# Kernel optimization log

Measured on AMD Instinct MI355X. Metric: run time of the kernel, lower is better.

## Reference

```python
import jax, jax.numpy as jnp
import numpy as np

N, E, D, H, C = 50000, 1600000, 128, 2, 32

def setup_inputs() -> dict:
    key = jax.random.key(0)
    ks = jax.random.split(key, 8)
    x = jax.random.normal(ks[0], (N, D), jnp.float32)
    edge_index = jax.random.randint(ks[1], (2, E), 0, N)
    intra_enrichment_weights = jax.random.uniform(ks[2], (E,), jnp.float32)
    W = jax.random.normal(ks[3], (D, H * C), jnp.float32) * (1.0 / np.sqrt(D))
    att_src = jax.random.normal(ks[4], (H, C), jnp.float32) * 0.1
    att_dst = jax.random.normal(ks[5], (H, C), jnp.float32) * 0.1
    bias = jnp.zeros((H * C,), jnp.float32)
    enrichment_scale = jnp.asarray(0.01, jnp.float32)
    return dict(x=x, edge_index=edge_index,
                intra_enrichment_weights=intra_enrichment_weights,
                W=W, att_src=att_src, att_dst=att_dst, bias=bias,
                enrichment_scale=enrichment_scale)

def reference(x, edge_index, intra_enrichment_weights, W, att_src, att_dst, bias, enrichment_scale):
    n = x.shape[0]
    xf = jax.nn.elu(x)                       # F.elu on input features
    h = (xf @ W).reshape(n, H, C)            # [N, heads, out]
    # GATConv default add_self_loops=True
    loop = jnp.arange(n, dtype=edge_index.dtype)
    src = jnp.concatenate([edge_index[0], loop])
    dst = jnp.concatenate([edge_index[1], loop])
    a_src = jnp.einsum('nhc,hc->nh', h, att_src)   # [N, H]
    a_dst = jnp.einsum('nhc,hc->nh', h, att_dst)
    alpha = jax.nn.leaky_relu(a_src[src] + a_dst[dst], 0.2)  # [E+N, H]
    # softmax over incoming edges per destination node
    m = jax.ops.segment_max(alpha, dst, num_segments=n)
    e = jnp.exp(alpha - m[dst])
    denom = jax.ops.segment_sum(e, dst, num_segments=n)
    p = e / denom[dst]                       # every node has a self-loop -> denom > 0
    out = jax.ops.segment_sum(h[src] * p[:, :, None], dst, num_segments=n)  # [N, H, C]
    out = out.reshape(n, H * C) + bias
    # enrichment bias (scatter-mean of per-edge weights over source nodes)
    s0 = edge_index[0]
    nw = jax.ops.segment_sum(intra_enrichment_weights, s0, num_segments=n)
    cnt = jax.ops.segment_sum(jnp.ones_like(intra_enrichment_weights), s0, num_segments=n)
    nw = nw / jnp.maximum(cnt, 1.0)
    nw = jnp.clip(nw, 0.2, 5.0)
    scale_factor = 0.1 * jax.nn.sigmoid(enrichment_scale)
    return out + scale_factor * (nw[:, None] - 1.0)
```

## Files before the change

kernel.cpp:

```cpp
#include <hip/hip_runtime.h>


typedef unsigned int u32;
typedef unsigned short u16;

#define SLOTS2 2624
#define NB2_MAX 800
#define EPB 4096

#define XS 136
#define CS 68

#define SMEM_F 34816

typedef __attribute__((ext_vector_type(8))) short short8;
typedef __attribute__((ext_vector_type(4))) float float4v;

__device__ __forceinline__ u16 f2bf(float f) {
    union { float f; u32 u; } v; v.f = f;
    u32 r = v.u + 0x7fffu + ((v.u >> 16) & 1u);
    return (u16)(r >> 16);
}
__device__ __forceinline__ float bf2f(u16 u) {
    union { u32 i; float f; } v; v.i = ((u32)u) << 16; return v.f;
}
__device__ __forceinline__ float bf_lo(u32 u) {
    union { u32 i; float f; } v; v.i = u << 16; return v.f;
}
__device__ __forceinline__ float bf_hi(u32 u) {
    union { u32 i; float f; } v; v.i = u & 0xFFFF0000u; return v.f;
}
__device__ __forceinline__ void bf_split(float v, short& hi, short& lo) {
    u16 h = f2bf(v);
    float hf = bf2f(h);
    hi = (short)h;
    lo = (short)f2bf(v - hf);
}

__global__ void k_prep(const float* __restrict__ Wm,
                       short* __restrict__ Whf, short* __restrict__ Wlf)
{
    int t = threadIdx.x;
    for (int p = t; p < 1024; p += 256) {
        int frag = p >> 6, l = p & 63;
        int ks = frag >> 2, nt = frag & 3;
        int q = l >> 4, m = l & 15;
        int f = nt * 16 + m;
#pragma unroll
        for (int j = 0; j < 8; ++j) {
            int k = ks * 32 + q * 8 + j;
            float wv = Wm[k * 64 + f];
            short hi, lo; bf_split(wv, hi, lo);
            Whf[p * 8 + j] = hi;
            Wlf[p * 8 + j] = lo;
        }
    }
}

static __device__ __forceinline__ void node_body(
    char* smem, int nb_id,
    const float* __restrict__ x,
    const short* __restrict__ Whf, const short* __restrict__ Wlf,
    const float* __restrict__ att_s, const float* __restrict__ att_d,
    u32* __restrict__ hb32, float* __restrict__ a_src, float* __restrict__ a_dst,
    int nN)
{
    short* Ah = (short*)smem;
    short* Al = (short*)(smem + 17408);
    float* Cl = (float*)Ah;

    int t = threadIdx.x;
    int n0 = nb_id * 64;

    for (int j = 0; j < 8; ++j) {
        int idx = t + 256 * j;
        int r = idx >> 5, c4 = idx & 31;
        int gn = n0 + r;
        float4 xv = make_float4(0.f, 0.f, 0.f, 0.f);
        if (gn < nN) xv = ((const float4*)x)[(size_t)gn * 32 + c4];
        float e[4];
        e[0] = xv.x > 0.f ? xv.x : __expf(xv.x) - 1.f;
        e[1] = xv.y > 0.f ? xv.y : __expf(xv.y) - 1.f;
        e[2] = xv.z > 0.f ? xv.z : __expf(xv.z) - 1.f;
        e[3] = xv.w > 0.f ? xv.w : __expf(xv.w) - 1.f;
        short h4[4], l4[4];
#pragma unroll
        for (int i = 0; i < 4; ++i) bf_split(e[i], h4[i], l4[i]);
        *(short4*)&Ah[r * XS + c4 * 4] = make_short4(h4[0], h4[1], h4[2], h4[3]);
        *(short4*)&Al[r * XS + c4 * 4] = make_short4(l4[0], l4[1], l4[2], l4[3]);
    }
    __syncthreads();

    {
        int w = t >> 6, l = t & 63;
        int q = l >> 4, m = l & 15;
        int arow = w * 16 + m;
        float4v acc[4] = {};
#pragma unroll
        for (int ks = 0; ks < 4; ++ks) {
            int k0 = ks * 32 + q * 8;
            short8 ah = *(const short8*)&Ah[arow * XS + k0];
            short8 al = *(const short8*)&Al[arow * XS + k0];
#pragma unroll
            for (int nt = 0; nt < 4; ++nt) {
                short8 bh = *(const short8*)&Whf[((ks * 4 + nt) * 64 + l) * 8];
                short8 bl = *(const short8*)&Wlf[((ks * 4 + nt) * 64 + l) * 8];
                acc[nt] = __builtin_amdgcn_mfma_f32_16x16x32_bf16(ah, bh, acc[nt], 0, 0, 0);
                acc[nt] = __builtin_amdgcn_mfma_f32_16x16x32_bf16(ah, bl, acc[nt], 0, 0, 0);
                acc[nt] = __builtin_amdgcn_mfma_f32_16x16x32_bf16(al, bh, acc[nt], 0, 0, 0);
            }
        }
        __syncthreads();
#pragma unroll
        for (int nt = 0; nt < 4; ++nt)
#pragma unroll
            for (int r = 0; r < 4; ++r)
                Cl[(w * 16 + q * 4 + r) * CS + nt * 16 + m] = acc[nt][r];
    }
    __syncthreads();

    {
        int nl = t >> 2, fq = t & 3;
        int gn = n0 + nl;
        float ps = 0.f, pd = 0.f;
        if (gn < nN) {
            float hv[16];
#pragma unroll
            for (int i = 0; i < 16; ++i) {
                int f = fq * 16 + i;
                hv[i] = Cl[nl * CS + f];
                ps = fmaf(hv[i], att_s[f], ps);
                pd = fmaf(hv[i], att_d[f], pd);
            }
#pragma unroll
            for (int i = 0; i < 8; ++i) {
                u32 pk = ((u32)f2bf(hv[2 * i + 1]) << 16) | (u32)f2bf(hv[2 * i]);
                hb32[(size_t)gn * 32 + fq * 8 + i] = pk;
            }
        }
        float ps2 = ps + __shfl_xor(ps, 1, 64);
        float pd2 = pd + __shfl_xor(pd, 1, 64);
        if (gn < nN && (fq & 1) == 0) {
            a_src[2 * gn + (fq >> 1)] = ps2;
            a_dst[2 * gn + (fq >> 1)] = pd2;
        }
    }
}

static __device__ __forceinline__ void partA_body(
    char* smem, int pa_id,
    const int* __restrict__ ei, const float* __restrict__ wgt,
    int* cursA, int* cursB, u32* bufA, u32* bufB, int E, int nb2)
{
    u32* arr  = (u32*)smem;
    int* cnt  = (int*)(smem + 16384);
    int* lofs = (int*)(smem + 19584);
    int* bas  = (int*)(smem + 22784);
    int* part = (int*)(smem + 25984);

    int t = threadIdx.x;
    int base = pa_id * EPB;
    int nv = min(EPB, E - base);
    int sv[16], dv[16]; float wv[16];
#pragma unroll
    for (int k = 0; k < 16; ++k) {
        int e = base + k * 256 + t;
        if (e < E) { sv[k] = ei[e]; dv[k] = ei[E + e]; wv[k] = wgt[e]; }
        else       { sv[k] = -1;    dv[k] = -1;        wv[k] = 0.f; }
    }

#pragma unroll
    for (int side = 0; side < 2; ++side) {
        int* curs = side ? cursB : cursA;
        u32* buf  = side ? bufB  : bufA;

        for (int b = t; b < nb2; b += 256) cnt[b] = 0;
        __syncthreads();
#pragma unroll
        for (int k = 0; k < 16; ++k) {
            int key = side ? sv[k] : dv[k];
            if (key >= 0) atomicAdd(&cnt[key >> 6], 1);
        }
        __syncthreads();
        for (int b = t; b < nb2; b += 256) {
            int c = cnt[b];
            if (c > 0) bas[b] = atomicAdd(&curs[b], c);
        }
        __syncthreads();
        {
            int c[4]; int s = 0;
#pragma unroll
            for (int i = 0; i < 4; ++i) {
                int bb = 4 * t + i;
                c[i] = (bb < nb2) ? cnt[bb] : 0;
                s += c[i];
            }
            part[t] = s;
            __syncthreads();
            for (int off = 1; off < 256; off <<= 1) {
                int v = (t >= off) ? part[t - off] : 0;
                __syncthreads();
                part[t] += v;
                __syncthreads();
            }
            int excl = part[t] - s;
#pragma unroll
            for (int i = 0; i < 4; ++i) {
                int bb = 4 * t + i;
                if (bb < nb2) lofs[bb] = excl;
                excl += c[i];
            }
        }
        __syncthreads();
        for (int b = t; b < nb2; b += 256) cnt[b] = 0;
        __syncthreads();
#pragma unroll
        for (int k = 0; k < 16; ++k) {
            int key = side ? sv[k] : dv[k];
            if (key >= 0) {
                int bk = key >> 6;
                int r = lofs[bk] + atomicAdd(&cnt[bk], 1);
                u32 payload;
                if (side) {
                    u32 wq = (u32)(wv[k] * 65536.f);
                    if (wq > 0xFFFFu) wq = 0xFFFFu;
                    payload = ((u32)(key & 63) << 16) | wq;
                } else {
                    payload = ((u32)(key & 63) << 16) | (u32)sv[k];
                }
                arr[r] = ((u32)bk << 22) | payload;
            }
        }
        __syncthreads();
        for (int i = t; i < nv; i += 256) {
            u32 va = arr[i];
            int bk = va >> 22;
            int g = bas[bk] + (i - lofs[bk]);
            if (g < SLOTS2) buf[(size_t)bk * SLOTS2 + g] = va & 0x3FFFFFu;
        }
        __syncthreads();
    }
}

__global__ __launch_bounds__(256) void k_fused(
    const float* __restrict__ x,
    const short* __restrict__ Whf, const short* __restrict__ Wlf,
    const float* __restrict__ att_s, const float* __restrict__ att_d,
    u32* __restrict__ hb32, float* __restrict__ a_src, float* __restrict__ a_dst,
    const int* __restrict__ ei, const float* __restrict__ wgt,
    int* cursA, int* cursB, u32* bufA, u32* bufB,
    int E, int nb2, int nblkA, int nN)
{
    __shared__ __align__(16) char smem[SMEM_F];
    int bid = blockIdx.x;
    int q3 = bid / 3;
    if ((bid % 3) == 0 && q3 < nblkA) {
        partA_body(smem, q3, ei, wgt, cursA, cursB, bufA, bufB, E, nb2);
    } else {
        int npa_before = min(q3 + ((bid % 3) ? 1 : 0), nblkA);
        node_body(smem, bid - npa_before, x, Whf, Wlf, att_s, att_d,
                  hb32, a_src, a_dst, nN);
    }
}

__global__ __launch_bounds__(512) void k_final(
    const u32* __restrict__ hb32,
    const float* __restrict__ a_src, const float* __restrict__ a_dst,
    const u32* __restrict__ bufA, const int* __restrict__ cursA,
    const u32* __restrict__ bufB, const int* __restrict__ cursB,
    const float* __restrict__ bias, const float* __restrict__ esc,
    float* __restrict__ out, int nN)
{
    __shared__ u32 st[SLOTS2];
    __shared__ u16 st2[SLOTS2];
    __shared__ int ldeg[64], lscan[64], lcur[64];
    __shared__ int usum[64], ucnt[64];

    int b = blockIdx.x, t = threadIdx.x;
    int n0 = b << 6;
    int nA = cursA[b]; if (nA > SLOTS2) nA = SLOTS2;
    int nB = cursB[b]; if (nB > SLOTS2) nB = SLOTS2;

    if (t < 64) { ldeg[t] = 0; lcur[t] = 0; usum[t] = 0; ucnt[t] = 0; }
    __syncthreads();
    for (int i = t; i < nA; i += 512) {
        u32 v = bufA[(size_t)b * SLOTS2 + i];
        st[i] = v;
        atomicAdd(&ldeg[v >> 16], 1);
    }
    for (int i = t; i < nB; i += 512) {
        u32 v = bufB[(size_t)b * SLOTS2 + i];
        atomicAdd(&usum[v >> 16], (int)(v & 0xFFFFu));
        atomicAdd(&ucnt[v >> 16], 1);
    }
    __syncthreads();
    if (t < 64) lscan[t] = ldeg[t];
    __syncthreads();
    for (int off = 1; off < 64; off <<= 1) {
        int v = 0;
        if (t < 64 && t >= off) v = lscan[t - off];
        __syncthreads();
        if (t < 64) lscan[t] += v;
        __syncthreads();
    }
    if (t < 64) lscan[t] -= ldeg[t];
    __syncthreads();
    for (int i = t; i < nA; i += 512) {
        u32 v = st[i];
        int dl = v >> 16;
        int pos = lscan[dl] + atomicAdd(&lcur[dl], 1);
        st2[pos] = (u16)(v & 0xFFFFu);
    }
    __syncthreads();

    int ws = t >> 6, lane = t & 63;
    int q = lane >> 4, fl = lane & 15, head = fl >> 3;
    const uint2* hb2 = (const uint2*)hb32;
    float escv = esc[0];
    float sf = 0.1f / (1.f + __expf(-escv));
    float4 bb = ((const float4*)bias)[fl];

    for (int dl = ws; dl < 64; dl += 8) {
        int gn = n0 + dl;
        if (gn >= nN) break;
        int beg = lscan[dl], cnt = ldeg[dl];
        float2 adv = ((const float2*)a_dst)[gn];
        float2 asv = ((const float2*)a_src)[gn];
        float t0 = asv.x + adv.x; t0 = t0 > 0.f ? t0 : 0.2f * t0;
        float t1 = asv.y + adv.y; t1 = t1 > 0.f ? t1 : 0.2f * t1;
        float es0 = __expf(t0), es1 = __expf(t1);

        float acc0 = 0.f, acc1 = 0.f, acc2 = 0.f, acc3 = 0.f;
        if (q == 0) {
            float eself = head ? es1 : es0;
            uint2 hs = hb2[(size_t)gn * 16 + fl];
            acc0 = eself * bf_lo(hs.x);
            acc1 = eself * bf_hi(hs.x);
            acc2 = eself * bf_lo(hs.y);
            acc3 = eself * bf_hi(hs.y);
        }
        float dsum0 = 0.f, dsum1 = 0.f;

        for (int b0 = 0; b0 < cnt; b0 += 64) {
            int wn = cnt - b0; if (wn > 64) wn = 64;
            u32 si = (u32)gn; float e0 = 0.f, e1 = 0.f;
            if (lane < wn) {
                si = (u32)st2[beg + b0 + lane];
                float2 ap = ((const float2*)a_src)[si];
                float v0 = ap.x + adv.x; v0 = v0 > 0.f ? v0 : 0.2f * v0;
                float v1 = ap.y + adv.y; v1 = v1 > 0.f ? v1 : 0.2f * v1;
                e0 = __expf(v0); e1 = __expf(v1);
            }
            dsum0 += e0; dsum1 += e1;

            int iters = (wn + 3) >> 2;
#pragma unroll 8
            for (int k = 0; k < iters; ++k) {
                int e = 4 * k + q;
                u32 rsi = __shfl(si, e, 64);
                uint2 hv = hb2[(size_t)rsi * 16 + fl];
                float w0 = __shfl(e0, e, 64);
                float w1 = __shfl(e1, e, 64);
                float w = head ? w1 : w0;
                acc0 = fmaf(w, bf_lo(hv.x), acc0);
                acc1 = fmaf(w, bf_hi(hv.x), acc1);
                acc2 = fmaf(w, bf_lo(hv.y), acc2);
                acc3 = fmaf(w, bf_hi(hv.y), acc3);
            }
        }
#pragma unroll
        for (int off = 1; off < 64; off <<= 1) {
            dsum0 += __shfl_xor(dsum0, off, 64);
            dsum1 += __shfl_xor(dsum1, off, 64);
        }
        acc0 += __shfl_xor(acc0, 16, 64); acc0 += __shfl_xor(acc0, 32, 64);
        acc1 += __shfl_xor(acc1, 16, 64); acc1 += __shfl_xor(acc1, 32, 64);
        acc2 += __shfl_xor(acc2, 16, 64); acc2 += __shfl_xor(acc2, 32, 64);
        acc3 += __shfl_xor(acc3, 16, 64); acc3 += __shfl_xor(acc3, 32, 64);

        if (q == 0) {
            float den = (head ? es1 : es0) + (head ? dsum1 : dsum0);
            float inv = 1.f / den;
            float cntf = (float)ucnt[dl];
            float nw = ((float)usum[dl] * (1.f / 65536.f)) / fmaxf(cntf, 1.f);
            nw = fminf(fmaxf(nw, 0.2f), 5.f);
            float en = sf * (nw - 1.f);
            float4 o;
            o.x = acc0 * inv + bb.x + en;
            o.y = acc1 * inv + bb.y + en;
            o.z = acc2 * inv + bb.z + en;
            o.w = acc3 * inv + bb.w + en;
            ((float4*)out)[(size_t)gn * 16 + fl] = o;
        }
    }
}

extern "C" void kernel_launch(void* const* d_in, const int* in_sizes, int n_in,
                              void* d_out, int out_size, void* d_ws, size_t ws_size,
                              hipStream_t stream)
{
    const float* x     = (const float*)d_in[0];
    const int*   ei    = (const int*)d_in[1];
    const float* wgt   = (const float*)d_in[2];
    const float* Wm    = (const float*)d_in[3];
    const float* att_s = (const float*)d_in[4];
    const float* att_d = (const float*)d_in[5];
    const float* bias  = (const float*)d_in[6];
    const float* esc   = (const float*)d_in[7];
    float* out = (float*)d_out;

    int nN = in_sizes[0] / 128;
    int E  = in_sizes[2];
    int NB2 = (nN + 63) / 64;

    char* p = (char*)d_ws;
    auto alloc = [&](size_t bytes) -> char* {
        char* r = p; p += (bytes + 255) & ~(size_t)255; return r;
    };
    u32*   hb32  = (u32*)  alloc((size_t)nN * 32 * 4);
    float* a_src = (float*)alloc((size_t)nN * 2 * 4);
    float* a_dst = (float*)alloc((size_t)nN * 2 * 4);
    short* Whf   = (short*)alloc(16 * 64 * 8 * 2);
    short* Wlf   = (short*)alloc(16 * 64 * 8 * 2);
    int*   cursA = (int*)  alloc(NB2_MAX * 4);
    int*   cursB = (int*)  alloc(NB2_MAX * 4);
    u32*   bufA  = (u32*)  alloc((size_t)NB2 * SLOTS2 * 4);
    u32*   bufB  = (u32*)  alloc((size_t)NB2 * SLOTS2 * 4);

    int nblkA = (E + EPB - 1) / EPB;
    int nblkN = (nN + 63) / 64;
    int nblkF = nblkA + nblkN;

    hipMemsetAsync(cursA, 0, (size_t)((char*)bufA - (char*)cursA), stream);
    k_prep<<<dim3(1), dim3(256), 0, stream>>>(Wm, Whf, Wlf);
    k_fused<<<dim3(nblkF), dim3(256), 0, stream>>>(x, Whf, Wlf, att_s, att_d,
                                                   hb32, a_src, a_dst,
                                                   ei, wgt, cursA, cursB, bufA, bufB,
                                                   E, NB2, nblkA, nN);
    k_final<<<dim3(NB2), dim3(512), 0, stream>>>(hb32, a_src, a_dst, bufA, cursA,
                                                 bufB, cursB, bias, esc, out, nN);
}
```

Before: 183.4 us.

## Process two destination nodes per wave concurrently in final aggregation, fold memset into prep

The final aggregation kernel now has each wave handle two destination nodes at once, interleaving their edge windows so two independent gather streams are in flight per iteration. The denominator sum is moved into the inner loop and reduced across only the q groups, replacing the full 64-lane butterfly reduction. The cursor memset is removed in favour of zeroing the cursors inside the prep kernel, which saves a separate memset launch. In exchange, register pressure roughly doubles and there is wasted work when the two nodes have very different degrees.

After: 177.8 us. 3.0% less time.

```diff
diff --git a/kernel.cpp b/kernel.cpp
--- a/kernel.cpp
+++ b/kernel.cpp
@@ -38,9 +38,11 @@
 }
 
 __global__ void k_prep(const float* __restrict__ Wm,
-                       short* __restrict__ Whf, short* __restrict__ Wlf)
+                       short* __restrict__ Whf, short* __restrict__ Wlf,
+                       int* cursA, int* cursB)
 {
     int t = threadIdx.x;
+    for (int i = t; i < NB2_MAX; i += 256) { cursA[i] = 0; cursB[i] = 0; }
     for (int p = t; p < 1024; p += 256) {
         int frag = p >> 6, l = p & 63;
         int ks = frag >> 2, nt = frag & 3;
@@ -320,77 +322,137 @@
     float sf = 0.1f / (1.f + __expf(-escv));
     float4 bb = ((const float4*)bias)[fl];
 
-    for (int dl = ws; dl < 64; dl += 8) {
-        int gn = n0 + dl;
-        if (gn >= nN) break;
-        int beg = lscan[dl], cnt = ldeg[dl];
-        float2 adv = ((const float2*)a_dst)[gn];
-        float2 asv = ((const float2*)a_src)[gn];
-        float t0 = asv.x + adv.x; t0 = t0 > 0.f ? t0 : 0.2f * t0;
-        float t1 = asv.y + adv.y; t1 = t1 > 0.f ? t1 : 0.2f * t1;
-        float es0 = __expf(t0), es1 = __expf(t1);
-
-        float acc0 = 0.f, acc1 = 0.f, acc2 = 0.f, acc3 = 0.f;
+    for (int dl0 = ws; dl0 < 64; dl0 += 16) {
+        int dlA = dl0, dlB = dl0 + 8;
+        int gnA = n0 + dlA, gnB = n0 + dlB;
+        if (gnA >= nN) break;
+        bool vB = (gnB < nN);
+
+        int begA = lscan[dlA], cntA = ldeg[dlA];
+        float2 advA = ((const float2*)a_dst)[gnA];
+        float2 asvA = ((const float2*)a_src)[gnA];
+        float tA0 = asvA.x + advA.x; tA0 = tA0 > 0.f ? tA0 : 0.2f * tA0;
+        float tA1 = asvA.y + advA.y; tA1 = tA1 > 0.f ? tA1 : 0.2f * tA1;
+        float esA0 = __expf(tA0), esA1 = __expf(tA1);
+        float aA0 = 0.f, aA1 = 0.f, aA2 = 0.f, aA3 = 0.f;
         if (q == 0) {
-            float eself = head ? es1 : es0;
-            uint2 hs = hb2[(size_t)gn * 16 + fl];
-            acc0 = eself * bf_lo(hs.x);
-            acc1 = eself * bf_hi(hs.x);
-            acc2 = eself * bf_lo(hs.y);
-            acc3 = eself * bf_hi(hs.y);
-        }
-        float dsum0 = 0.f, dsum1 = 0.f;
-
-        for (int b0 = 0; b0 < cnt; b0 += 64) {
-            int wn = cnt - b0; if (wn > 64) wn = 64;
-            u32 si = (u32)gn; float e0 = 0.f, e1 = 0.f;
-            if (lane < wn) {
-                si = (u32)st2[beg + b0 + lane];
-                float2 ap = ((const float2*)a_src)[si];
-                float v0 = ap.x + adv.x; v0 = v0 > 0.f ? v0 : 0.2f * v0;
-                float v1 = ap.y + adv.y; v1 = v1 > 0.f ? v1 : 0.2f * v1;
-                e0 = __expf(v0); e1 = __expf(v1);
-            }
-            dsum0 += e0; dsum1 += e1;
-
-            int iters = (wn + 3) >> 2;
-#pragma unroll 8
+            float eself = head ? esA1 : esA0;
+            uint2 hs = hb2[(size_t)gnA * 16 + fl];
+            aA0 = eself * bf_lo(hs.x); aA1 = eself * bf_hi(hs.x);
+            aA2 = eself * bf_lo(hs.y); aA3 = eself * bf_hi(hs.y);
+        }
+        float dsA = 0.f;
+
+        int begB = 0, cntB = 0;
+        float2 advB = make_float2(0.f, 0.f);
+        float esB0 = 0.f, esB1 = 0.f;
+        float aB0 = 0.f, aB1 = 0.f, aB2 = 0.f, aB3 = 0.f;
+        float dsB = 0.f;
+        if (vB) {
+            begB = lscan[dlB]; cntB = ldeg[dlB];
+            advB = ((const float2*)a_dst)[gnB];
+            float2 asvB = ((const float2*)a_src)[gnB];
+            float tB0 = asvB.x + advB.x; tB0 = tB0 > 0.f ? tB0 : 0.2f * tB0;
+            float tB1 = asvB.y + advB.y; tB1 = tB1 > 0.f ? tB1 : 0.2f * tB1;
+            esB0 = __expf(tB0); esB1 = __expf(tB1);
+            if (q == 0) {
+                float eself = head ? esB1 : esB0;
+                uint2 hs = hb2[(size_t)gnB * 16 + fl];
+                aB0 = eself * bf_lo(hs.x); aB1 = eself * bf_hi(hs.x);
+                aB2 = eself * bf_lo(hs.y); aB3 = eself * bf_hi(hs.y);
+            }
+        }
+
+        int nwA = (cntA + 63) >> 6, nwB = (cntB + 63) >> 6;
+        int nwin = nwA > nwB ? nwA : nwB;
+        for (int w = 0; w < nwin; ++w) {
+            int b0 = w << 6;
+            u32 siA = (u32)gnA; float eA0 = 0.f, eA1 = 0.f; int wnA = 0;
+            if (w < nwA) {
+                wnA = cntA - b0; if (wnA > 64) wnA = 64;
+                if (lane < wnA) {
+                    siA = (u32)st2[begA + b0 + lane];
+                    float2 ap = ((const float2*)a_src)[siA];
+                    float v0 = ap.x + advA.x; v0 = v0 > 0.f ? v0 : 0.2f * v0;
+                    float v1 = ap.y + advA.y; v1 = v1 > 0.f ? v1 : 0.2f * v1;
+                    eA0 = __expf(v0); eA1 = __expf(v1);
+                }
+            }
+            u32 siB = (u32)gnA; float eB0 = 0.f, eB1 = 0.f; int wnB = 0;
+            if (w < nwB) {
+                wnB = cntB - b0; if (wnB > 64) wnB = 64;
+                if (lane < wnB) {
+                    siB = (u32)st2[begB + b0 + lane];
+                    float2 ap = ((const float2*)a_src)[siB];
+                    float v0 = ap.x + advB.x; v0 = v0 > 0.f ? v0 : 0.2f * v0;
+                    float v1 = ap.y + advB.y; v1 = v1 > 0.f ? v1 : 0.2f * v1;
+                    eB0 = __expf(v0); eB1 = __expf(v1);
+                }
+            }
+            int wmax = wnA > wnB ? wnA : wnB;
+            int iters = (wmax + 3) >> 2;
+#pragma unroll 4
             for (int k = 0; k < iters; ++k) {
                 int e = 4 * k + q;
-                u32 rsi = __shfl(si, e, 64);
-                uint2 hv = hb2[(size_t)rsi * 16 + fl];
-                float w0 = __shfl(e0, e, 64);
-                float w1 = __shfl(e1, e, 64);
-                float w = head ? w1 : w0;
-                acc0 = fmaf(w, bf_lo(hv.x), acc0);
-                acc1 = fmaf(w, bf_hi(hv.x), acc1);
-                acc2 = fmaf(w, bf_lo(hv.y), acc2);
-                acc3 = fmaf(w, bf_hi(hv.y), acc3);
-            }
-        }
-#pragma unroll
-        for (int off = 1; off < 64; off <<= 1) {
-            dsum0 += __shfl_xor(dsum0, off, 64);
-            dsum1 += __shfl_xor(dsum1, off, 64);
-        }
-        acc0 += __shfl_xor(acc0, 16, 64); acc0 += __shfl_xor(acc0, 32, 64);
-        acc1 += __shfl_xor(acc1, 16, 64); acc1 += __shfl_xor(acc1, 32, 64);
-        acc2 += __shfl_xor(acc2, 16, 64); acc2 += __shfl_xor(acc2, 32, 64);
-        acc3 += __shfl_xor(acc3, 16, 64); acc3 += __shfl_xor(acc3, 32, 64);
+                u32 rsiA = __shfl(siA, e, 64);
+                u32 rsiB = __shfl(siB, e, 64);
+                uint2 hvA = hb2[(size_t)rsiA * 16 + fl];
+                uint2 hvB = hb2[(size_t)rsiB * 16 + fl];
+                float w0A = __shfl(eA0, e, 64), w1A = __shfl(eA1, e, 64);
+                float w0B = __shfl(eB0, e, 64), w1B = __shfl(eB1, e, 64);
+                float wA = head ? w1A : w0A;
+                float wB = head ? w1B : w0B;
+                dsA += wA; dsB += wB;
+                aA0 = fmaf(wA, bf_lo(hvA.x), aA0);
+                aA1 = fmaf(wA, bf_hi(hvA.x), aA1);
+                aA2 = fmaf(wA, bf_lo(hvA.y), aA2);
+                aA3 = fmaf(wA, bf_hi(hvA.y), aA3);
+                aB0 = fmaf(wB, bf_lo(hvB.x), aB0);
+                aB1 = fmaf(wB, bf_hi(hvB.x), aB1);
+                aB2 = fmaf(wB, bf_lo(hvB.y), aB2);
+                aB3 = fmaf(wB, bf_hi(hvB.y), aB3);
+            }
+        }
+        dsA += __shfl_xor(dsA, 16, 64); dsA += __shfl_xor(dsA, 32, 64);
+        dsB += __shfl_xor(dsB, 16, 64); dsB += __shfl_xor(dsB, 32, 64);
+        aA0 += __shfl_xor(aA0, 16, 64); aA0 += __shfl_xor(aA0, 32, 64);
+        aA1 += __shfl_xor(aA1, 16, 64); aA1 += __shfl_xor(aA1, 32, 64);
+        aA2 += __shfl_xor(aA2, 16, 64); aA2 += __shfl_xor(aA2, 32, 64);
+        aA3 += __shfl_xor(aA3, 16, 64); aA3 += __shfl_xor(aA3, 32, 64);
+        aB0 += __shfl_xor(aB0, 16, 64); aB0 += __shfl_xor(aB0, 32, 64);
+        aB1 += __shfl_xor(aB1, 16, 64); aB1 += __shfl_xor(aB1, 32, 64);
+        aB2 += __shfl_xor(aB2, 16, 64); aB2 += __shfl_xor(aB2, 32, 64);
+        aB3 += __shfl_xor(aB3, 16, 64); aB3 += __shfl_xor(aB3, 32, 64);
 
         if (q == 0) {
-            float den = (head ? es1 : es0) + (head ? dsum1 : dsum0);
-            float inv = 1.f / den;
-            float cntf = (float)ucnt[dl];
-            float nw = ((float)usum[dl] * (1.f / 65536.f)) / fmaxf(cntf, 1.f);
-            nw = fminf(fmaxf(nw, 0.2f), 5.f);
-            float en = sf * (nw - 1.f);
-            float4 o;
-            o.x = acc0 * inv + bb.x + en;
-            o.y = acc1 * inv + bb.y + en;
-            o.z = acc2 * inv + bb.z + en;
-            o.w = acc3 * inv + bb.w + en;
-            ((float4*)out)[(size_t)gn * 16 + fl] = o;
+            {
+                float den = (head ? esA1 : esA0) + dsA;
+                float inv = 1.f / den;
+                float cntf = (float)ucnt[dlA];
+                float nw = ((float)usum[dlA] * (1.f / 65536.f)) / fmaxf(cntf, 1.f);
+                nw = fminf(fmaxf(nw, 0.2f), 5.f);
+                float en = sf * (nw - 1.f);
+                float4 o;
+                o.x = aA0 * inv + bb.x + en;
+                o.y = aA1 * inv + bb.y + en;
+                o.z = aA2 * inv + bb.z + en;
+                o.w = aA3 * inv + bb.w + en;
+                ((float4*)out)[(size_t)gnA * 16 + fl] = o;
+            }
+            if (vB) {
+                float den = (head ? esB1 : esB0) + dsB;
+                float inv = 1.f / den;
+                float cntf = (float)ucnt[dlB];
+                float nw = ((float)usum[dlB] * (1.f / 65536.f)) / fmaxf(cntf, 1.f);
+                nw = fminf(fmaxf(nw, 0.2f), 5.f);
+                float en = sf * (nw - 1.f);
+                float4 o;
+                o.x = aB0 * inv + bb.x + en;
+                o.y = aB1 * inv + bb.y + en;
+                o.z = aB2 * inv + bb.z + en;
+                o.w = aB3 * inv + bb.w + en;
+                ((float4*)out)[(size_t)gnB * 16 + fl] = o;
+            }
         }
     }
 }
@@ -431,8 +493,7 @@
     int nblkN = (nN + 63) / 64;
     int nblkF = nblkA + nblkN;
 
-    hipMemsetAsync(cursA, 0, (size_t)((char*)bufA - (char*)cursA), stream);
-    k_prep<<<dim3(1), dim3(256), 0, stream>>>(Wm, Whf, Wlf);
+    k_prep<<<dim3(1), dim3(256), 0, stream>>>(Wm, Whf, Wlf, cursA, cursB);
     k_fused<<<dim3(nblkF), dim3(256), 0, stream>>>(x, Whf, Wlf, att_s, att_d,
                                                    hb32, a_src, a_dst,
                                                    ei, wgt, cursA, cursB, bufA, bufB,
```
